# Optimization experiments

Hardware: AMD Instinct MI355X
Metric: run time of the kernel (lower is better)

Reference implementation:

```python
import jax, jax.numpy as jnp
import numpy as np

D_MODEL = 256
N_HEADS = 8
N_LEVELS = 4
N_POINTS = 4
HEAD_DIM = D_MODEL // N_HEADS
SPATIAL = [(64, 64), (32, 32), (16, 16), (8, 8)]
LEN_IN = sum(h * w for h, w in SPATIAL)
BATCH = 4
LEN_Q = LEN_IN


def _offset_bias():
    # replicate the module's _reset_parameters grid init for sampling_offsets.bias
    th = np.arange(N_HEADS, dtype=np.float64) * (2.0 * np.pi / N_HEADS)
    g = np.stack([np.cos(th), np.sin(th)], -1)
    g = g / np.abs(g).max(-1, keepdims=True)
    g = np.tile(g[:, None, None, :], (1, N_LEVELS, N_POINTS, 1))
    g = g * (np.arange(N_POINTS) + 1)[None, None, :, None]
    return jnp.asarray(g.reshape(-1), jnp.float32)


def setup_inputs() -> dict:
    key = jax.random.key(0)
    ks = jax.random.split(key, 10)
    s = 1.0 / np.sqrt(D_MODEL)
    return {
        "query": jax.random.normal(ks[0], (BATCH, LEN_Q, D_MODEL), jnp.float32),
        "reference_points": jax.random.uniform(ks[1], (BATCH, LEN_Q, N_LEVELS, 2), jnp.float32),
        "input_flatten": jax.random.normal(ks[2], (BATCH, LEN_IN, D_MODEL), jnp.float32),
        "input_spatial_shapes": np.array(SPATIAL, dtype=np.int64),
        "input_level_start_index": np.cumsum([0] + [h * w for h, w in SPATIAL[:-1]]).astype(np.int64),
        "W_val": jax.random.normal(ks[3], (D_MODEL, D_MODEL), jnp.float32) * s,
        "b_val": jnp.zeros((D_MODEL,), jnp.float32),
        "W_off": jax.random.normal(ks[4], (D_MODEL, N_HEADS * N_LEVELS * N_POINTS * 2), jnp.float32) * 0.01,
        "b_off": _offset_bias(),
        "W_attn": jax.random.normal(ks[5], (D_MODEL, N_HEADS * N_LEVELS * N_POINTS), jnp.float32) * 0.01,
        "b_attn": jnp.zeros((N_HEADS * N_LEVELS * N_POINTS,), jnp.float32),
        "W_out": jax.random.normal(ks[6], (D_MODEL, D_MODEL), jnp.float32) * s,
        "b_out": jnp.zeros((D_MODEL,), jnp.float32),
    }


def bilinear_sample(v, grid):
    # v: [B, C, H, W]; grid: [B, Q, P, 2] normalized to [-1, 1] (x=W axis, y=H axis)
    # matches torch F.grid_sample(mode='bilinear', padding_mode='zeros', align_corners=False)
    B, C, H, W = v.shape
    x = (grid[..., 0] + 1.0) * (W * 0.5) - 0.5
    y = (grid[..., 1] + 1.0) * (H * 0.5) - 0.5
    x0 = jnp.floor(x)
    y0 = jnp.floor(y)
    wx = x - x0
    wy = y - y0
    v_flat = v.reshape(B, C, H * W)

    def corner(xi, yi, wgt):
        valid = (xi >= 0) & (xi <= W - 1) & (yi >= 0) & (yi <= H - 1)
        xc = jnp.clip(xi, 0, W - 1).astype(jnp.int32)
        yc = jnp.clip(yi, 0, H - 1).astype(jnp.int32)
        idx = (yc * W + xc).reshape(B, 1, -1)
        g = jnp.take_along_axis(v_flat, jnp.broadcast_to(idx, (B, C, idx.shape[-1])), axis=2)
        return g * (wgt * valid).reshape(B, 1, -1)

    out = (corner(x0, y0, (1 - wx) * (1 - wy))
           + corner(x0 + 1, y0, wx * (1 - wy))
           + corner(x0, y0 + 1, (1 - wx) * wy)
           + corner(x0 + 1, y0 + 1, wx * wy))
    return out.reshape(B, C, grid.shape[1], grid.shape[2])


def reference(query, reference_points, input_flatten, input_spatial_shapes,
              input_level_start_index, W_val, b_val, W_off, b_off,
              W_attn, b_attn, W_out, b_out):
    ss = np.asarray(input_spatial_shapes)  # static [L, 2] (H, W)
    Nb, Lq, _ = query.shape
    value = (input_flatten @ W_val + b_val).reshape(Nb, -1, N_HEADS, HEAD_DIM)
    off = (query @ W_off + b_off).reshape(Nb, Lq, N_HEADS, N_LEVELS, N_POINTS, 2)
    attn = (query @ W_attn + b_attn).reshape(Nb, Lq, N_HEADS, N_LEVELS * N_POINTS)
    attn = jax.nn.softmax(attn, -1).reshape(Nb, Lq, N_HEADS, N_LEVELS, N_POINTS)
    # offset normalizer: (W, H) per level
    normalizer = jnp.asarray(ss[:, ::-1].copy(), jnp.float32)
    loc = reference_points[:, :, None, :, None, :] + off / normalizer[None, None, None, :, None, :]
    grids = 2.0 * loc - 1.0  # [N, Lq, H, L, P, 2]
    splits = np.cumsum([int(h) * int(w) for h, w in ss])[:-1]
    value_list = jnp.split(value, splits, axis=1)
    out = jnp.zeros((Nb * N_HEADS, HEAD_DIM, Lq), query.dtype)
    for lid, (h, w) in enumerate(ss):
        h, w = int(h), int(w)
        v = value_list[lid].transpose(0, 2, 3, 1).reshape(Nb * N_HEADS, HEAD_DIM, h, w)
        g = grids[:, :, :, lid].transpose(0, 2, 1, 3, 4).reshape(Nb * N_HEADS, Lq, N_POINTS, 2)
        sampled = bilinear_sample(v, g)  # [N*H, D, Lq, P]
        aw = attn[:, :, :, lid].transpose(0, 2, 1, 3).reshape(Nb * N_HEADS, 1, Lq, N_POINTS)
        out = out + (sampled * aw).sum(-1)
    out = out.reshape(Nb, N_HEADS * HEAD_DIM, Lq).transpose(0, 2, 1)
    return out @ W_out + b_out
```

## Files before the change

### kernel.cpp

```cpp
#include <hip/hip_runtime.h>
#include <hip/hip_bf16.h>
#include <math.h>

typedef unsigned short ushort_t;
typedef __attribute__((ext_vector_type(8))) short bf16x8;
typedef __attribute__((ext_vector_type(4))) float f32x4;

constexpr int BATCH   = 4;
constexpr int D_MODEL = 256;
constexpr int LEN_IN  = 5440;
constexpr int LEN_Q   = 5440;
constexpr int M_TOT   = BATCH * LEN_Q;

#define ASG __attribute__((address_space(1)))
#define ASL __attribute__((address_space(3)))

__device__ __forceinline__ void gld16(const void* g, void* l) {
    __builtin_amdgcn_global_load_lds((ASG const void*)g, (ASL void*)l, 16, 0, 0);
}

__device__ __forceinline__ ushort_t bfbits(float x) {
    __hip_bfloat16 h = __float2bfloat16(x);
    ushort_t u; __builtin_memcpy(&u, &h, 2); return u;
}
__device__ __forceinline__ unsigned pk2(float a, float b) {
    return (unsigned)bfbits(a) | ((unsigned)bfbits(b) << 16);
}

__global__ __launch_bounds__(256) void pack_inputs(
    const float* __restrict__ inflat, const float* __restrict__ query,
    const float* __restrict__ Wv, const float* __restrict__ Wo,
    const float* __restrict__ Wa, const float* __restrict__ Wout,
    const float* __restrict__ b_off, const float* __restrict__ b_attn,
    ushort_t* __restrict__ in_bf, ushort_t* __restrict__ q_bf,
    ushort_t* __restrict__ wvT, ushort_t* __restrict__ woaT,
    ushort_t* __restrict__ woutT, float* __restrict__ bias_oa)
{
    const int blk = blockIdx.x, tid = threadIdx.x;
    if (blk < 5440) {
        const float* src = (blk < 2720) ? inflat : query;
        ushort_t*    dst = (blk < 2720) ? in_bf : q_bf;
        const int rb = (blk < 2720) ? blk : blk - 2720;
        const size_t base = (size_t)rb * 2048 + tid * 8;
        float4 a = *(const float4*)(src + base);
        float4 b = *(const float4*)(src + base + 4);
        uint4 o;
        o.x = pk2(a.x, a.y); o.y = pk2(a.z, a.w);
        o.z = pk2(b.x, b.y); o.w = pk2(b.z, b.w);
        *(uint4*)(dst + base) = o;
    } else if (blk < 5504) {
        const float* src = (blk < 5472) ? Wv : Wout;
        ushort_t*    dst = (blk < 5472) ? wvT : woutT;
        const int base = (blk - ((blk < 5472) ? 5440 : 5472)) * 2048;
#pragma unroll
        for (int i = 0; i < 8; i++) {
            const int idx = base + i * 256 + tid;
            const int k = idx >> 8, n = idx & 255;
            dst[n * 256 + k] = bfbits(src[idx]);
        }
    } else if (blk < 5552) {
        const int base = (blk - 5504) * 2048;
#pragma unroll
        for (int i = 0; i < 8; i++) {
            const int idx = base + i * 256 + tid;
            const int k = idx / 384, j = idx - k * 384;
            const float v = (j < 256) ? Wo[k * 256 + j] : Wa[k * 128 + (j - 256)];
            woaT[j * 256 + k] = bfbits(v);
        }
    } else {
        bias_oa[tid] = b_off[tid];
        if (tid < 128) bias_oa[256 + tid] = b_attn[tid];
    }
}

template <bool OUT_BF16>
__device__ __forceinline__ void gemm_core(
    const ushort_t* __restrict__ A, const ushort_t* __restrict__ BT,
    const float* __restrict__ bias, void* __restrict__ Cp, int N,
    int bm, int bn, ushort_t* As, ushort_t* Bs)
{
    const int tid  = threadIdx.x;
    const int wave = tid >> 6, lane = tid & 63;
    const int wm = (wave >> 1) * 64, wn = (wave & 1) * 64;
    const int c0 = 2 * wave, c1 = 2 * wave + 1;
    const int kb = (lane & 3) * 8;
    const ushort_t* gA0 = A  + (size_t)(bm + c0 * 16 + (lane >> 2)) * 256 + kb;
    const ushort_t* gA1 = A  + (size_t)(bm + c1 * 16 + (lane >> 2)) * 256 + kb;
    const ushort_t* gB0 = BT + (size_t)(bn + c0 * 16 + (lane >> 2)) * 256 + kb;
    const ushort_t* gB1 = BT + (size_t)(bn + c1 * 16 + (lane >> 2)) * 256 + kb;
    ushort_t* lA0 = As + c0 * 512;
    ushort_t* lA1 = As + c1 * 512;
    ushort_t* lB0 = Bs + c0 * 512;
    ushort_t* lB1 = Bs + c1 * 512;

    f32x4 acc[4][4] = {};

    const int row = lane & 15, kg = (lane >> 4) * 8;
    for (int kt = 0; kt < 8; kt++) {
        gld16(gA0, lA0); gld16(gA1, lA1);
        gld16(gB0, lB0); gld16(gB1, lB1);
        gA0 += 32; gA1 += 32; gB0 += 32; gB1 += 32;
        __syncthreads();
        bf16x8 af[4], bfr[4];
#pragma unroll
        for (int i = 0; i < 4; i++)
            af[i] = *(const bf16x8*)(As + (wm + i * 16 + row) * 32 + kg);
#pragma unroll
        for (int j = 0; j < 4; j++)
            bfr[j] = *(const bf16x8*)(Bs + (wn + j * 16 + row) * 32 + kg);
#pragma unroll
        for (int i = 0; i < 4; i++)
#pragma unroll
            for (int j = 0; j < 4; j++)
                acc[i][j] = __builtin_amdgcn_mfma_f32_16x16x32_bf16(
                    af[i], bfr[j], acc[i][j], 0, 0, 0);
        __syncthreads();
    }

    const int col = lane & 15, rbase = (lane >> 4) * 4;
#pragma unroll
    for (int j = 0; j < 4; j++) {
        const int cc = bn + wn + j * 16 + col;
        const float bv = bias[cc];
#pragma unroll
        for (int i = 0; i < 4; i++) {
            const int rr = bm + wm + i * 16 + rbase;
#pragma unroll
            for (int r = 0; r < 4; r++) {
                const float v = acc[i][j][r] + bv;
                if (OUT_BF16) ((ushort_t*)Cp)[(size_t)(rr + r) * N + cc] = bfbits(v);
                else          ((float*)Cp)[(size_t)(rr + r) * N + cc] = v;
            }
        }
    }
}

__global__ __launch_bounds__(256) void gemm_dual(
    const ushort_t* __restrict__ in_bf, const ushort_t* __restrict__ wvT,
    const float* __restrict__ b_val, ushort_t* __restrict__ value_bf,
    const ushort_t* __restrict__ q_bf, const ushort_t* __restrict__ woaT,
    const float* __restrict__ bias_oa, float* __restrict__ offattn)
{
    __shared__ ushort_t As[128 * 32];
    __shared__ ushort_t Bs[128 * 32];
    int blk = blockIdx.x;
    if (blk < 340) {
        const int bn = (blk & 1) * 128, bm = (blk >> 1) * 128;
        gemm_core<true>(in_bf, wvT, b_val, value_bf, 256, bm, bn, As, Bs);
    } else {
        blk -= 340;
        const int bn = (blk % 3) * 128, bm = (blk / 3) * 128;
        gemm_core<false>(q_bf, woaT, bias_oa, offattn, 384, bm, bn, As, Bs);
    }
}

__global__ __launch_bounds__(256) void gemm_out(
    const ushort_t* __restrict__ mid_bf, const ushort_t* __restrict__ woutT,
    const float* __restrict__ b_out, float* __restrict__ out)
{
    __shared__ ushort_t As[128 * 32];
    __shared__ ushort_t Bs[128 * 32];
    const int bn = (blockIdx.x & 1) * 128, bm = (blockIdx.x >> 1) * 128;
    gemm_core<false>(mid_bf, woutT, b_out, out, 256, bm, bn, As, Bs);
}

__device__ __forceinline__ void acc8(float* acc, uint4 v, float w) {
    const unsigned* p = &v.x;
#pragma unroll
    for (int d = 0; d < 4; d++) {
        const unsigned u = p[d];
        const float lo = __uint_as_float(u << 16);
        const float hi = __uint_as_float(u & 0xFFFF0000u);
        acc[2 * d]     = fmaf(w, lo, acc[2 * d]);
        acc[2 * d + 1] = fmaf(w, hi, acc[2 * d + 1]);
    }
}

__global__ __launch_bounds__(256) void msda_sample_bf16(
    const ushort_t* __restrict__ value, const float* __restrict__ refp,
    const float* __restrict__ offattn, ushort_t* __restrict__ mid)
{
    constexpr int LVL_H[4]  = {64, 32, 16, 8};
    constexpr int LVL_W[4]  = {64, 32, 16, 8};
    constexpr int LVL_ST[4] = {0, 4096, 5120, 5376};

    const int tid  = threadIdx.x;
    const int bq   = blockIdx.x * 8 + (tid >> 5);
    const int b    = bq / LEN_Q;
    const int t32  = tid & 31;
    const int head = t32 >> 2;
    const int c8   = (t32 & 3) * 8;

    const float* base = offattn + (size_t)bq * 384;
    const float* lp = base + 256 + head * 16;
    float4 l0 = ((const float4*)lp)[0];
    float4 l1 = ((const float4*)lp)[1];
    float4 l2 = ((const float4*)lp)[2];
    float4 l3 = ((const float4*)lp)[3];
    float lg[16] = {l0.x, l0.y, l0.z, l0.w, l1.x, l1.y, l1.z, l1.w,
                    l2.x, l2.y, l2.z, l2.w, l3.x, l3.y, l3.z, l3.w};
    float mx = lg[0];
#pragma unroll
    for (int j = 1; j < 16; j++) mx = fmaxf(mx, lg[j]);

    const float* op = base + head * 32;
    float4 ov[8];
#pragma unroll
    for (int j = 0; j < 8; j++) ov[j] = ((const float4*)op)[j];
    const float* rp = refp + (size_t)bq * 8;
    float4 r0 = ((const float4*)rp)[0];
    float4 r1 = ((const float4*)rp)[1];
    const float rx[4] = {r0.x, r0.z, r1.x, r1.z};
    const float ry[4] = {r0.y, r0.w, r1.y, r1.w};

    const ushort_t* vbase = value + (size_t)b * LEN_IN * 256 + head * 32 + c8;

    float acc[8] = {};
    float esum = 0.f;

#pragma unroll
    for (int l = 0; l < 4; l++) {
        const int H = LVL_H[l], W = LVL_W[l], st = LVL_ST[l];
        const float fW = (float)W, fH = (float)H;
#pragma unroll
        for (int p = 0; p < 4; p++) {
            const float* o2 = &ov[l * 2].x;
            const float ox = o2[p * 2 + 0];
            const float oy = o2[p * 2 + 1];
            const float x = (rx[l] + ox / fW) * fW - 0.5f;
            const float y = (ry[l] + oy / fH) * fH - 0.5f;
            const float x0f = floorf(x), y0f = floorf(y);
            const float wx = x - x0f, wy = y - y0f;
            const int ix0 = (int)x0f, iy0 = (int)y0f;
            const int ix1 = ix0 + 1,  iy1 = iy0 + 1;
            const float vx0 = (ix0 >= 0 && ix0 < W) ? 1.f : 0.f;
            const float vx1 = (ix1 >= 0 && ix1 < W) ? 1.f : 0.f;
            const float vy0 = (iy0 >= 0 && iy0 < H) ? 1.f : 0.f;
            const float vy1 = (iy1 >= 0 && iy1 < H) ? 1.f : 0.f;
            const int cx0 = min(max(ix0, 0), W - 1);
            const int cx1 = min(max(ix1, 0), W - 1);
            const int cy0 = min(max(iy0, 0), H - 1);
            const int cy1 = min(max(iy1, 0), H - 1);
            const float hx0 = (1.f - wx) * vx0, hx1 = wx * vx1;
            const float hy0 = (1.f - wy) * vy0, hy1 = wy * vy1;

            const ushort_t* rp0 = vbase + (size_t)(st + cy0 * W) * 256;
            const ushort_t* rp1 = vbase + (size_t)(st + cy1 * W) * 256;
            uint4 v00 = *(const uint4*)(rp0 + (size_t)cx0 * 256);
            uint4 v01 = *(const uint4*)(rp0 + (size_t)cx1 * 256);
            uint4 v10 = *(const uint4*)(rp1 + (size_t)cx0 * 256);
            uint4 v11 = *(const uint4*)(rp1 + (size_t)cx1 * 256);

            const float e = __expf(lg[l * 4 + p] - mx);
            esum += e;
            acc8(acc, v00, e * hx0 * hy0);
            acc8(acc, v01, e * hx1 * hy0);
            acc8(acc, v10, e * hx0 * hy1);
            acc8(acc, v11, e * hx1 * hy1);
        }
    }

    const float inv = 1.f / esum;
    uint4 o;
    o.x = pk2(acc[0] * inv, acc[1] * inv);
    o.y = pk2(acc[2] * inv, acc[3] * inv);
    o.z = pk2(acc[4] * inv, acc[5] * inv);
    o.w = pk2(acc[6] * inv, acc[7] * inv);
    *(uint4*)(mid + (size_t)bq * 256 + head * 32 + c8) = o;
}

extern "C" void kernel_launch(void* const* d_in, const int* in_sizes, int n_in,
                              void* d_out, int out_size, void* d_ws, size_t ws_size,
                              hipStream_t stream)
{
    const float* query  = (const float*)d_in[0];
    const float* refp   = (const float*)d_in[1];
    const float* inflat = (const float*)d_in[2];
    const float* W_val  = (const float*)d_in[5];
    const float* b_val  = (const float*)d_in[6];
    const float* W_off  = (const float*)d_in[7];
    const float* W_attn = (const float*)d_in[9];
    const float* b_off  = (const float*)d_in[8];
    const float* b_attn = (const float*)d_in[10];
    const float* W_out  = (const float*)d_in[11];
    const float* b_out  = (const float*)d_in[12];
    float* out = (float*)d_out;

    char* ws = (char*)d_ws;
    ushort_t* in_bf    = (ushort_t*)ws;
    ushort_t* q_bf     = (ushort_t*)(ws + 11141120);
    ushort_t* value_bf = (ushort_t*)(ws + 22282240);
    ushort_t* wvT      = (ushort_t*)(ws + 33423360);
    ushort_t* woutT    = (ushort_t*)(ws + 33554432);
    ushort_t* woaT     = (ushort_t*)(ws + 33685504);
    float*    bias_oa  = (float*)   (ws + 33882112);
    float*    offattn  = (float*)   (ws + 33883648);
    ushort_t* mid_bf   = in_bf;

    dim3 blk(256);
    pack_inputs<<<dim3(5553), blk, 0, stream>>>(
        inflat, query, W_val, W_off, W_attn, W_out, b_off, b_attn,
        in_bf, q_bf, wvT, woaT, woutT, bias_oa);
    gemm_dual<<<dim3(850), blk, 0, stream>>>(
        in_bf, wvT, b_val, value_bf, q_bf, woaT, bias_oa, offattn);
    msda_sample_bf16<<<dim3(M_TOT / 8), blk, 0, stream>>>(
        value_bf, refp, offattn, mid_bf);
    gemm_out<<<dim3(340), blk, 0, stream>>>(
        mid_bf, woutT, b_out, out);
}
```

Before: 206.1 us.

## Fuse fp32-to-bf16 input conversion into GEMM loads, stage epilogue, prefetch samples

Drops the separate pass that converted input_flatten and query to bf16. The projection GEMM now reads the fp32 activations directly and converts them in registers before storing to LDS, using plain loads in place of global_load_lds. The GEMM epilogue is staged through LDS so each lane writes contiguous 16-element rows with vector stores, instead of scattered scalar stores. The sampling kernel is software-pipelined so the next point's four corner loads are issued before the current point is accumulated. In exchange, the GEMM reads twice as many bytes of A and uses more synchronisation barriers per tile.

```diff
diff --git a/kernel.cpp b/kernel.cpp
--- a/kernel.cpp
+++ b/kernel.cpp
@@ -7,18 +7,10 @@
 typedef __attribute__((ext_vector_type(4))) float f32x4;
 
 constexpr int BATCH   = 4;
-constexpr int D_MODEL = 256;
 constexpr int LEN_IN  = 5440;
 constexpr int LEN_Q   = 5440;
 constexpr int M_TOT   = BATCH * LEN_Q;
 
-#define ASG __attribute__((address_space(1)))
-#define ASL __attribute__((address_space(3)))
-
-__device__ __forceinline__ void gld16(const void* g, void* l) {
-    __builtin_amdgcn_global_load_lds((ASG const void*)g, (ASL void*)l, 16, 0, 0);
-}
-
 __device__ __forceinline__ ushort_t bfbits(float x) {
     __hip_bfloat16 h = __float2bfloat16(x);
     ushort_t u; __builtin_memcpy(&u, &h, 2); return u;
@@ -27,39 +19,26 @@
     return (unsigned)bfbits(a) | ((unsigned)bfbits(b) << 16);
 }
 
-__global__ __launch_bounds__(256) void pack_inputs(
-    const float* __restrict__ inflat, const float* __restrict__ query,
+__global__ __launch_bounds__(256) void pack_w(
     const float* __restrict__ Wv, const float* __restrict__ Wo,
     const float* __restrict__ Wa, const float* __restrict__ Wout,
     const float* __restrict__ b_off, const float* __restrict__ b_attn,
-    ushort_t* __restrict__ in_bf, ushort_t* __restrict__ q_bf,
     ushort_t* __restrict__ wvT, ushort_t* __restrict__ woaT,
     ushort_t* __restrict__ woutT, float* __restrict__ bias_oa)
 {
     const int blk = blockIdx.x, tid = threadIdx.x;
-    if (blk < 5440) {
-        const float* src = (blk < 2720) ? inflat : query;
-        ushort_t*    dst = (blk < 2720) ? in_bf : q_bf;
-        const int rb = (blk < 2720) ? blk : blk - 2720;
-        const size_t base = (size_t)rb * 2048 + tid * 8;
-        float4 a = *(const float4*)(src + base);
-        float4 b = *(const float4*)(src + base + 4);
-        uint4 o;
-        o.x = pk2(a.x, a.y); o.y = pk2(a.z, a.w);
-        o.z = pk2(b.x, b.y); o.w = pk2(b.z, b.w);
-        *(uint4*)(dst + base) = o;
-    } else if (blk < 5504) {
-        const float* src = (blk < 5472) ? Wv : Wout;
-        ushort_t*    dst = (blk < 5472) ? wvT : woutT;
-        const int base = (blk - ((blk < 5472) ? 5440 : 5472)) * 2048;
+    if (blk < 64) {
+        const float* src = (blk < 32) ? Wv : Wout;
+        ushort_t*    dst = (blk < 32) ? wvT : woutT;
+        const int base = (blk & 31) * 2048;
 #pragma unroll
         for (int i = 0; i < 8; i++) {
             const int idx = base + i * 256 + tid;
             const int k = idx >> 8, n = idx & 255;
             dst[n * 256 + k] = bfbits(src[idx]);
         }
-    } else if (blk < 5552) {
-        const int base = (blk - 5504) * 2048;
+    } else if (blk < 112) {
+        const int base = (blk - 64) * 2048;
 #pragma unroll
         for (int i = 0; i < 8; i++) {
             const int idx = base + i * 256 + tid;
@@ -73,84 +52,123 @@
     }
 }
 
-template <bool OUT_BF16>
+template <bool A_F32, bool OUT_BF16>
 __device__ __forceinline__ void gemm_core(
-    const ushort_t* __restrict__ A, const ushort_t* __restrict__ BT,
+    const void* __restrict__ Ap, const ushort_t* __restrict__ BT,
     const float* __restrict__ bias, void* __restrict__ Cp, int N,
-    int bm, int bn, ushort_t* As, ushort_t* Bs)
-{
+    int bm, int bn, ushort_t* SMEM)
+{
+    ushort_t* As = SMEM;
+    ushort_t* Bs = SMEM + 4096;
     const int tid  = threadIdx.x;
     const int wave = tid >> 6, lane = tid & 63;
     const int wm = (wave >> 1) * 64, wn = (wave & 1) * 64;
-    const int c0 = 2 * wave, c1 = 2 * wave + 1;
-    const int kb = (lane & 3) * 8;
-    const ushort_t* gA0 = A  + (size_t)(bm + c0 * 16 + (lane >> 2)) * 256 + kb;
-    const ushort_t* gA1 = A  + (size_t)(bm + c1 * 16 + (lane >> 2)) * 256 + kb;
-    const ushort_t* gB0 = BT + (size_t)(bn + c0 * 16 + (lane >> 2)) * 256 + kb;
-    const ushort_t* gB1 = BT + (size_t)(bn + c1 * 16 + (lane >> 2)) * 256 + kb;
-    ushort_t* lA0 = As + c0 * 512;
-    ushort_t* lA1 = As + c1 * 512;
-    ushort_t* lB0 = Bs + c0 * 512;
-    ushort_t* lB1 = Bs + c1 * 512;
+    const int srow = tid >> 1, skh = (tid & 1) * 16;
+    const int row16 = lane & 15, kg = (lane >> 4) * 8;
 
     f32x4 acc[4][4] = {};
 
-    const int row = lane & 15, kg = (lane >> 4) * 8;
     for (int kt = 0; kt < 8; kt++) {
-        gld16(gA0, lA0); gld16(gA1, lA1);
-        gld16(gB0, lB0); gld16(gB1, lB1);
-        gA0 += 32; gA1 += 32; gB0 += 32; gB1 += 32;
+        const int k0 = kt * 32;
+        uint4 a0, a1;
+        if (A_F32) {
+            const float* ap = (const float*)Ap + (size_t)(bm + srow) * 256 + k0 + skh;
+            float4 f0 = *(const float4*)(ap);
+            float4 f1 = *(const float4*)(ap + 4);
+            float4 f2 = *(const float4*)(ap + 8);
+            float4 f3 = *(const float4*)(ap + 12);
+            a0.x = pk2(f0.x, f0.y); a0.y = pk2(f0.z, f0.w);
+            a0.z = pk2(f1.x, f1.y); a0.w = pk2(f1.z, f1.w);
+            a1.x = pk2(f2.x, f2.y); a1.y = pk2(f2.z, f2.w);
+            a1.z = pk2(f3.x, f3.y); a1.w = pk2(f3.z, f3.w);
+        } else {
+            const ushort_t* ap = (const ushort_t*)Ap + (size_t)(bm + srow) * 256 + k0 + skh;
+            a0 = ((const uint4*)ap)[0];
+            a1 = ((const uint4*)ap)[1];
+        }
+        const ushort_t* bp = BT + (size_t)(bn + srow) * 256 + k0 + skh;
+        uint4 b0 = ((const uint4*)bp)[0];
+        uint4 b1 = ((const uint4*)bp)[1];
+        __syncthreads();
+        *(uint4*)(As + srow * 32 + skh)     = a0;
+        *(uint4*)(As + srow * 32 + skh + 8) = a1;
+        *(uint4*)(Bs + srow * 32 + skh)     = b0;
+        *(uint4*)(Bs + srow * 32 + skh + 8) = b1;
         __syncthreads();
         bf16x8 af[4], bfr[4];
 #pragma unroll
         for (int i = 0; i < 4; i++)
-            af[i] = *(const bf16x8*)(As + (wm + i * 16 + row) * 32 + kg);
+            af[i] = *(const bf16x8*)(As + (wm + i * 16 + row16) * 32 + kg);
 #pragma unroll
         for (int j = 0; j < 4; j++)
-            bfr[j] = *(const bf16x8*)(Bs + (wn + j * 16 + row) * 32 + kg);
+            bfr[j] = *(const bf16x8*)(Bs + (wn + j * 16 + row16) * 32 + kg);
 #pragma unroll
         for (int i = 0; i < 4; i++)
 #pragma unroll
             for (int j = 0; j < 4; j++)
                 acc[i][j] = __builtin_amdgcn_mfma_f32_16x16x32_bf16(
                     af[i], bfr[j], acc[i][j], 0, 0, 0);
+    }
+
+    float* sw = (float*)SMEM + wave * (16 * 68);
+    const int rb4 = (lane >> 4) * 4;
+    float bv[4];
+#pragma unroll
+    for (int j = 0; j < 4; j++) bv[j] = bias[bn + wn + j * 16 + row16];
+    const int err = lane >> 2;
+    const int ecs = (lane & 3) * 16;
+
+#pragma unroll
+    for (int i = 0; i < 4; i++) {
         __syncthreads();
-    }
-
-    const int col = lane & 15, rbase = (lane >> 4) * 4;
-#pragma unroll
-    for (int j = 0; j < 4; j++) {
-        const int cc = bn + wn + j * 16 + col;
-        const float bv = bias[cc];
-#pragma unroll
-        for (int i = 0; i < 4; i++) {
-            const int rr = bm + wm + i * 16 + rbase;
-#pragma unroll
-            for (int r = 0; r < 4; r++) {
-                const float v = acc[i][j][r] + bv;
-                if (OUT_BF16) ((ushort_t*)Cp)[(size_t)(rr + r) * N + cc] = bfbits(v);
-                else          ((float*)Cp)[(size_t)(rr + r) * N + cc] = v;
-            }
+#pragma unroll
+        for (int j = 0; j < 4; j++)
+#pragma unroll
+            for (int r = 0; r < 4; r++)
+                sw[(rb4 + r) * 68 + j * 16 + row16] = acc[i][j][r] + bv[j];
+        __syncthreads();
+        const float* rp = sw + err * 68 + ecs;
+        f32x4 v0 = ((const f32x4*)rp)[0];
+        f32x4 v1 = ((const f32x4*)rp)[1];
+        f32x4 v2 = ((const f32x4*)rp)[2];
+        f32x4 v3 = ((const f32x4*)rp)[3];
+        const int grow = bm + wm + i * 16 + err;
+        if (OUT_BF16) {
+            ushort_t* cp = (ushort_t*)Cp + (size_t)grow * N + bn + wn + ecs;
+            uint4 o0, o1;
+            o0.x = pk2(v0[0], v0[1]); o0.y = pk2(v0[2], v0[3]);
+            o0.z = pk2(v1[0], v1[1]); o0.w = pk2(v1[2], v1[3]);
+            o1.x = pk2(v2[0], v2[1]); o1.y = pk2(v2[2], v2[3]);
+            o1.z = pk2(v3[0], v3[1]); o1.w = pk2(v3[2], v3[3]);
+            ((uint4*)cp)[0] = o0;
+            ((uint4*)cp)[1] = o1;
+        } else {
+            float* cp = (float*)Cp + (size_t)grow * N + bn + wn + ecs;
+            ((f32x4*)cp)[0] = v0;
+            ((f32x4*)cp)[1] = v1;
+            ((f32x4*)cp)[2] = v2;
+            ((f32x4*)cp)[3] = v3;
         }
     }
 }
 
+constexpr int SMEM_USHORTS = 4 * 16 * 68 * 2;
+
 __global__ __launch_bounds__(256) void gemm_dual(
-    const ushort_t* __restrict__ in_bf, const ushort_t* __restrict__ wvT,
+    const float* __restrict__ inflat, const ushort_t* __restrict__ wvT,
     const float* __restrict__ b_val, ushort_t* __restrict__ value_bf,
-    const ushort_t* __restrict__ q_bf, const ushort_t* __restrict__ woaT,
+    const float* __restrict__ query, const ushort_t* __restrict__ woaT,
     const float* __restrict__ bias_oa, float* __restrict__ offattn)
 {
-    __shared__ ushort_t As[128 * 32];
-    __shared__ ushort_t Bs[128 * 32];
+    __shared__ ushort_t SMEM[SMEM_USHORTS];
     int blk = blockIdx.x;
     if (blk < 340) {
         const int bn = (blk & 1) * 128, bm = (blk >> 1) * 128;
-        gemm_core<true>(in_bf, wvT, b_val, value_bf, 256, bm, bn, As, Bs);
+        gemm_core<true, true>(inflat, wvT, b_val, value_bf, 256, bm, bn, SMEM);
     } else {
         blk -= 340;
         const int bn = (blk % 3) * 128, bm = (blk / 3) * 128;
-        gemm_core<false>(q_bf, woaT, bias_oa, offattn, 384, bm, bn, As, Bs);
+        gemm_core<true, false>(query, woaT, bias_oa, offattn, 384, bm, bn, SMEM);
     }
 }
 
@@ -158,10 +176,9 @@
     const ushort_t* __restrict__ mid_bf, const ushort_t* __restrict__ woutT,
     const float* __restrict__ b_out, float* __restrict__ out)
 {
-    __shared__ ushort_t As[128 * 32];
-    __shared__ ushort_t Bs[128 * 32];
+    __shared__ ushort_t SMEM[SMEM_USHORTS];
     const int bn = (blockIdx.x & 1) * 128, bm = (blockIdx.x >> 1) * 128;
-    gemm_core<false>(mid_bf, woutT, b_out, out, 256, bm, bn, As, Bs);
+    gemm_core<false, false>(mid_bf, woutT, b_out, out, 256, bm, bn, SMEM);
 }
 
 __device__ __forceinline__ void acc8(float* acc, uint4 v, float w) {
@@ -218,46 +235,62 @@
     float acc[8] = {};
     float esum = 0.f;
 
-#pragma unroll
-    for (int l = 0; l < 4; l++) {
+    int   A00[2], A01[2], A10[2], A11[2];
+    float W00[2], W01[2], W10[2], W11[2];
+    uint4 V00[2], V01[2], V10[2], V11[2];
+
+    auto comp = [&](int pi) {
+        const int s = pi & 1;
+        const int l = pi >> 2, p = pi & 3;
         const int H = LVL_H[l], W = LVL_W[l], st = LVL_ST[l];
         const float fW = (float)W, fH = (float)H;
-#pragma unroll
-        for (int p = 0; p < 4; p++) {
-            const float* o2 = &ov[l * 2].x;
-            const float ox = o2[p * 2 + 0];
-            const float oy = o2[p * 2 + 1];
-            const float x = (rx[l] + ox / fW) * fW - 0.5f;
-            const float y = (ry[l] + oy / fH) * fH - 0.5f;
-            const float x0f = floorf(x), y0f = floorf(y);
-            const float wx = x - x0f, wy = y - y0f;
-            const int ix0 = (int)x0f, iy0 = (int)y0f;
-            const int ix1 = ix0 + 1,  iy1 = iy0 + 1;
-            const float vx0 = (ix0 >= 0 && ix0 < W) ? 1.f : 0.f;
-            const float vx1 = (ix1 >= 0 && ix1 < W) ? 1.f : 0.f;
-            const float vy0 = (iy0 >= 0 && iy0 < H) ? 1.f : 0.f;
-            const float vy1 = (iy1 >= 0 && iy1 < H) ? 1.f : 0.f;
-            const int cx0 = min(max(ix0, 0), W - 1);
-            const int cx1 = min(max(ix1, 0), W - 1);
-            const int cy0 = min(max(iy0, 0), H - 1);
-            const int cy1 = min(max(iy1, 0), H - 1);
-            const float hx0 = (1.f - wx) * vx0, hx1 = wx * vx1;
-            const float hy0 = (1.f - wy) * vy0, hy1 = wy * vy1;
-
-            const ushort_t* rp0 = vbase + (size_t)(st + cy0 * W) * 256;
-            const ushort_t* rp1 = vbase + (size_t)(st + cy1 * W) * 256;
-            uint4 v00 = *(const uint4*)(rp0 + (size_t)cx0 * 256);
-            uint4 v01 = *(const uint4*)(rp0 + (size_t)cx1 * 256);
-            uint4 v10 = *(const uint4*)(rp1 + (size_t)cx0 * 256);
-            uint4 v11 = *(const uint4*)(rp1 + (size_t)cx1 * 256);
-
-            const float e = __expf(lg[l * 4 + p] - mx);
-            esum += e;
-            acc8(acc, v00, e * hx0 * hy0);
-            acc8(acc, v01, e * hx1 * hy0);
-            acc8(acc, v10, e * hx0 * hy1);
-            acc8(acc, v11, e * hx1 * hy1);
-        }
+        const float* o2 = &ov[l * 2].x;
+        const float ox = o2[p * 2 + 0];
+        const float oy = o2[p * 2 + 1];
+        const float x = (rx[l] + ox / fW) * fW - 0.5f;
+        const float y = (ry[l] + oy / fH) * fH - 0.5f;
+        const float x0f = floorf(x), y0f = floorf(y);
+        const float wx = x - x0f, wy = y - y0f;
+        const int ix0 = (int)x0f, iy0 = (int)y0f;
+        const int ix1 = ix0 + 1,  iy1 = iy0 + 1;
+        const float vx0 = (ix0 >= 0 && ix0 < W) ? 1.f : 0.f;
+        const float vx1 = (ix1 >= 0 && ix1 < W) ? 1.f : 0.f;
+        const float vy0 = (iy0 >= 0 && iy0 < H) ? 1.f : 0.f;
+        const float vy1 = (iy1 >= 0 && iy1 < H) ? 1.f : 0.f;
+        const int cx0 = min(max(ix0, 0), W - 1);
+        const int cx1 = min(max(ix1, 0), W - 1);
+        const int cy0 = min(max(iy0, 0), H - 1);
+        const int cy1 = min(max(iy1, 0), H - 1);
+        const float hx0 = (1.f - wx) * vx0, hx1 = wx * vx1;
+        const float hy0 = (1.f - wy) * vy0, hy1 = wy * vy1;
+        const int r0i = (st + cy0 * W) * 256;
+        const int r1i = (st + cy1 * W) * 256;
+        A00[s] = r0i + cx0 * 256;
+        A01[s] = r0i + cx1 * 256;
+        A10[s] = r1i + cx0 * 256;
+        A11[s] = r1i + cx1 * 256;
+        const float e = __expf(lg[pi] - mx);
+        esum += e;
+        W00[s] = e * hx0 * hy0; W01[s] = e * hx1 * hy0;
+        W10[s] = e * hx0 * hy1; W11[s] = e * hx1 * hy1;
+    };
+    auto load = [&](int pi) {
+        const int s = pi & 1;
+        V00[s] = *(const uint4*)(vbase + A00[s]);
+        V01[s] = *(const uint4*)(vbase + A01[s]);
+        V10[s] = *(const uint4*)(vbase + A10[s]);
+        V11[s] = *(const uint4*)(vbase + A11[s]);
+    };
+
+    comp(0); load(0);
+#pragma unroll
+    for (int pi = 0; pi < 16; pi++) {
+        if (pi < 15) { comp(pi + 1); load(pi + 1); }
+        const int s = pi & 1;
+        acc8(acc, V00[s], W00[s]);
+        acc8(acc, V01[s], W01[s]);
+        acc8(acc, V10[s], W10[s]);
+        acc8(acc, V11[s], W11[s]);
     }
 
     const float inv = 1.f / esum;
@@ -279,30 +312,27 @@
     const float* W_val  = (const float*)d_in[5];
     const float* b_val  = (const float*)d_in[6];
     const float* W_off  = (const float*)d_in[7];
+    const float* b_off  = (const float*)d_in[8];
     const float* W_attn = (const float*)d_in[9];
-    const float* b_off  = (const float*)d_in[8];
     const float* b_attn = (const float*)d_in[10];
     const float* W_out  = (const float*)d_in[11];
     const float* b_out  = (const float*)d_in[12];
     float* out = (float*)d_out;
 
     char* ws = (char*)d_ws;
-    ushort_t* in_bf    = (ushort_t*)ws;
-    ushort_t* q_bf     = (ushort_t*)(ws + 11141120);
-    ushort_t* value_bf = (ushort_t*)(ws + 22282240);
-    ushort_t* wvT      = (ushort_t*)(ws + 33423360);
-    ushort_t* woutT    = (ushort_t*)(ws + 33554432);
-    ushort_t* woaT     = (ushort_t*)(ws + 33685504);
-    float*    bias_oa  = (float*)   (ws + 33882112);
-    float*    offattn  = (float*)   (ws + 33883648);
-    ushort_t* mid_bf   = in_bf;
+    ushort_t* value_bf = (ushort_t*)ws;
+    ushort_t* mid_bf   = (ushort_t*)(ws + 11141120);
+    float*    offattn  = (float*)   (ws + 22282240);
+    ushort_t* wvT      = (ushort_t*)(ws + 55705600);
+    ushort_t* woutT    = (ushort_t*)(ws + 55836672);
+    ushort_t* woaT     = (ushort_t*)(ws + 55967744);
+    float*    bias_oa  = (float*)   (ws + 56164352);
 
     dim3 blk(256);
-    pack_inputs<<<dim3(5553), blk, 0, stream>>>(
-        inflat, query, W_val, W_off, W_attn, W_out, b_off, b_attn,
-        in_bf, q_bf, wvT, woaT, woutT, bias_oa);
+    pack_w<<<dim3(113), blk, 0, stream>>>(
+        W_val, W_off, W_attn, W_out, b_off, b_attn, wvT, woaT, woutT, bias_oa);
     gemm_dual<<<dim3(850), blk, 0, stream>>>(
-        in_bf, wvT, b_val, value_bf, q_bf, woaT, bias_oa, offattn);
+        inflat, wvT, b_val, value_bf, query, woaT, bias_oa, offattn);
     msda_sample_bf16<<<dim3(M_TOT / 8), blk, 0, stream>>>(
         value_bf, refp, offattn, mid_bf);
     gemm_out<<<dim3(340), blk, 0, stream>>>(
```

Measured after the change: 221.5 us. +7.5%, slower.

## Fuse fp32-to-bf16 input conversion into register-resident single-wave GEMMs

Applied to the files above, without the earlier changes.

Drops the separate pass that packed the query and input tensors to bf16, so the projection GEMMs now read fp32 activations directly and convert them in registers. The LDS-tiled 256-thread GEMM is replaced by one-wave blocks that keep a 64-column slice of the weight matrix in registers as MFMA fragments and stream over 8 row tiles. This removes a full read and write of both activation tensors and all LDS traffic and barriers. In exchange each wave reloads its weight slice, register pressure is high (two waves per SIMD requested), and the A rows are read uncoalesced from global memory.

```diff
diff --git a/kernel.cpp b/kernel.cpp
--- a/kernel.cpp
+++ b/kernel.cpp
@@ -7,18 +7,10 @@
 typedef __attribute__((ext_vector_type(4))) float f32x4;
 
 constexpr int BATCH   = 4;
-constexpr int D_MODEL = 256;
 constexpr int LEN_IN  = 5440;
 constexpr int LEN_Q   = 5440;
 constexpr int M_TOT   = BATCH * LEN_Q;
 
-#define ASG __attribute__((address_space(1)))
-#define ASL __attribute__((address_space(3)))
-
-__device__ __forceinline__ void gld16(const void* g, void* l) {
-    __builtin_amdgcn_global_load_lds((ASG const void*)g, (ASL void*)l, 16, 0, 0);
-}
-
 __device__ __forceinline__ ushort_t bfbits(float x) {
     __hip_bfloat16 h = __float2bfloat16(x);
     ushort_t u; __builtin_memcpy(&u, &h, 2); return u;
@@ -27,39 +19,26 @@
     return (unsigned)bfbits(a) | ((unsigned)bfbits(b) << 16);
 }
 
-__global__ __launch_bounds__(256) void pack_inputs(
-    const float* __restrict__ inflat, const float* __restrict__ query,
+__global__ __launch_bounds__(256) void pack_w(
     const float* __restrict__ Wv, const float* __restrict__ Wo,
     const float* __restrict__ Wa, const float* __restrict__ Wout,
     const float* __restrict__ b_off, const float* __restrict__ b_attn,
-    ushort_t* __restrict__ in_bf, ushort_t* __restrict__ q_bf,
     ushort_t* __restrict__ wvT, ushort_t* __restrict__ woaT,
     ushort_t* __restrict__ woutT, float* __restrict__ bias_oa)
 {
     const int blk = blockIdx.x, tid = threadIdx.x;
-    if (blk < 5440) {
-        const float* src = (blk < 2720) ? inflat : query;
-        ushort_t*    dst = (blk < 2720) ? in_bf : q_bf;
-        const int rb = (blk < 2720) ? blk : blk - 2720;
-        const size_t base = (size_t)rb * 2048 + tid * 8;
-        float4 a = *(const float4*)(src + base);
-        float4 b = *(const float4*)(src + base + 4);
-        uint4 o;
-        o.x = pk2(a.x, a.y); o.y = pk2(a.z, a.w);
-        o.z = pk2(b.x, b.y); o.w = pk2(b.z, b.w);
-        *(uint4*)(dst + base) = o;
-    } else if (blk < 5504) {
-        const float* src = (blk < 5472) ? Wv : Wout;
-        ushort_t*    dst = (blk < 5472) ? wvT : woutT;
-        const int base = (blk - ((blk < 5472) ? 5440 : 5472)) * 2048;
+    if (blk < 64) {
+        const float* src = (blk < 32) ? Wv : Wout;
+        ushort_t*    dst = (blk < 32) ? wvT : woutT;
+        const int base = (blk & 31) * 2048;
 #pragma unroll
         for (int i = 0; i < 8; i++) {
             const int idx = base + i * 256 + tid;
             const int k = idx >> 8, n = idx & 255;
             dst[n * 256 + k] = bfbits(src[idx]);
         }
-    } else if (blk < 5552) {
-        const int base = (blk - 5504) * 2048;
+    } else if (blk < 112) {
+        const int base = (blk - 64) * 2048;
 #pragma unroll
         for (int i = 0; i < 8; i++) {
             const int idx = base + i * 256 + tid;
@@ -73,95 +52,100 @@
     }
 }
 
-template <bool OUT_BF16>
-__device__ __forceinline__ void gemm_core(
-    const ushort_t* __restrict__ A, const ushort_t* __restrict__ BT,
+constexpr int MC = 8;
+
+template <bool A_F32, bool OUT_BF16>
+__device__ __forceinline__ void gemm_wave(
+    const void* __restrict__ Ap, const ushort_t* __restrict__ BT,
     const float* __restrict__ bias, void* __restrict__ Cp, int N,
-    int bm, int bn, ushort_t* As, ushort_t* Bs)
-{
-    const int tid  = threadIdx.x;
-    const int wave = tid >> 6, lane = tid & 63;
-    const int wm = (wave >> 1) * 64, wn = (wave & 1) * 64;
-    const int c0 = 2 * wave, c1 = 2 * wave + 1;
-    const int kb = (lane & 3) * 8;
-    const ushort_t* gA0 = A  + (size_t)(bm + c0 * 16 + (lane >> 2)) * 256 + kb;
-    const ushort_t* gA1 = A  + (size_t)(bm + c1 * 16 + (lane >> 2)) * 256 + kb;
-    const ushort_t* gB0 = BT + (size_t)(bn + c0 * 16 + (lane >> 2)) * 256 + kb;
-    const ushort_t* gB1 = BT + (size_t)(bn + c1 * 16 + (lane >> 2)) * 256 + kb;
-    ushort_t* lA0 = As + c0 * 512;
-    ushort_t* lA1 = As + c1 * 512;
-    ushort_t* lB0 = Bs + c0 * 512;
-    ushort_t* lB1 = Bs + c1 * 512;
-
-    f32x4 acc[4][4] = {};
-
-    const int row = lane & 15, kg = (lane >> 4) * 8;
-    for (int kt = 0; kt < 8; kt++) {
-        gld16(gA0, lA0); gld16(gA1, lA1);
-        gld16(gB0, lB0); gld16(gB1, lB1);
-        gA0 += 32; gA1 += 32; gB0 += 32; gB1 += 32;
-        __syncthreads();
-        bf16x8 af[4], bfr[4];
-#pragma unroll
-        for (int i = 0; i < 4; i++)
-            af[i] = *(const bf16x8*)(As + (wm + i * 16 + row) * 32 + kg);
-#pragma unroll
-        for (int j = 0; j < 4; j++)
-            bfr[j] = *(const bf16x8*)(Bs + (wn + j * 16 + row) * 32 + kg);
-#pragma unroll
-        for (int i = 0; i < 4; i++)
-#pragma unroll
-            for (int j = 0; j < 4; j++)
-                acc[i][j] = __builtin_amdgcn_mfma_f32_16x16x32_bf16(
-                    af[i], bfr[j], acc[i][j], 0, 0, 0);
-        __syncthreads();
-    }
-
-    const int col = lane & 15, rbase = (lane >> 4) * 4;
-#pragma unroll
-    for (int j = 0; j < 4; j++) {
-        const int cc = bn + wn + j * 16 + col;
-        const float bv = bias[cc];
-#pragma unroll
-        for (int i = 0; i < 4; i++) {
-            const int rr = bm + wm + i * 16 + rbase;
+    int n0, int row_base)
+{
+    const int lane  = threadIdx.x & 63;
+    const int row16 = lane & 15;
+    const int kg8   = (lane >> 4) * 8;
+    const int rb4   = (lane >> 4) * 4;
+
+    bf16x8 Bf[4][8];
+#pragma unroll
+    for (int nt = 0; nt < 4; nt++)
+#pragma unroll
+        for (int kt = 0; kt < 8; kt++)
+            Bf[nt][kt] = *(const bf16x8*)(BT + (size_t)(n0 + nt * 16 + row16) * 256
+                                             + kt * 32 + kg8);
+    float bv[4];
+#pragma unroll
+    for (int nt = 0; nt < 4; nt++) bv[nt] = bias[n0 + nt * 16 + row16];
+
+#pragma unroll 1
+    for (int mt = 0; mt < MC; mt++) {
+        const int row0 = row_base + mt * 16;
+        bf16x8 af[8];
+        if (A_F32) {
+            const float* ap = (const float*)Ap + (size_t)(row0 + row16) * 256 + kg8;
+#pragma unroll
+            for (int kt = 0; kt < 8; kt++) {
+                float4 f0 = *(const float4*)(ap + kt * 32);
+                float4 f1 = *(const float4*)(ap + kt * 32 + 4);
+                uint4 u;
+                u.x = pk2(f0.x, f0.y); u.y = pk2(f0.z, f0.w);
+                u.z = pk2(f1.x, f1.y); u.w = pk2(f1.z, f1.w);
+                __builtin_memcpy(&af[kt], &u, 16);
+            }
+        } else {
+            const ushort_t* ap = (const ushort_t*)Ap + (size_t)(row0 + row16) * 256 + kg8;
+#pragma unroll
+            for (int kt = 0; kt < 8; kt++)
+                af[kt] = *(const bf16x8*)(ap + kt * 32);
+        }
+
+        f32x4 acc[4] = {};
+#pragma unroll
+        for (int kt = 0; kt < 8; kt++)
+#pragma unroll
+            for (int nt = 0; nt < 4; nt++)
+                acc[nt] = __builtin_amdgcn_mfma_f32_16x16x32_bf16(
+                    af[kt], Bf[nt][kt], acc[nt], 0, 0, 0);
+
+#pragma unroll
+        for (int nt = 0; nt < 4; nt++) {
+            const int cc = n0 + nt * 16 + row16;
 #pragma unroll
             for (int r = 0; r < 4; r++) {
-                const float v = acc[i][j][r] + bv;
-                if (OUT_BF16) ((ushort_t*)Cp)[(size_t)(rr + r) * N + cc] = bfbits(v);
-                else          ((float*)Cp)[(size_t)(rr + r) * N + cc] = v;
+                const float v = acc[nt][r] + bv[nt];
+                const size_t ci = (size_t)(row0 + rb4 + r) * N + cc;
+                if (OUT_BF16) ((ushort_t*)Cp)[ci] = bfbits(v);
+                else          ((float*)Cp)[ci] = v;
             }
         }
     }
 }
 
-__global__ __launch_bounds__(256) void gemm_dual(
-    const ushort_t* __restrict__ in_bf, const ushort_t* __restrict__ wvT,
+__global__ __launch_bounds__(64, 2) void gemm_vo(
+    const float* __restrict__ inflat, const ushort_t* __restrict__ wvT,
     const float* __restrict__ b_val, ushort_t* __restrict__ value_bf,
-    const ushort_t* __restrict__ q_bf, const ushort_t* __restrict__ woaT,
+    const float* __restrict__ query, const ushort_t* __restrict__ woaT,
     const float* __restrict__ bias_oa, float* __restrict__ offattn)
 {
-    __shared__ ushort_t As[128 * 32];
-    __shared__ ushort_t Bs[128 * 32];
-    int blk = blockIdx.x;
-    if (blk < 340) {
-        const int bn = (blk & 1) * 128, bm = (blk >> 1) * 128;
-        gemm_core<true>(in_bf, wvT, b_val, value_bf, 256, bm, bn, As, Bs);
+    int j = blockIdx.x;
+    if (j < 680) {
+        const int s = j & 3, chunk = j >> 2;
+        gemm_wave<true, true>(inflat, wvT, b_val, value_bf, 256,
+                              s * 64, chunk * (MC * 16));
     } else {
-        blk -= 340;
-        const int bn = (blk % 3) * 128, bm = (blk / 3) * 128;
-        gemm_core<false>(q_bf, woaT, bias_oa, offattn, 384, bm, bn, As, Bs);
-    }
-}
-
-__global__ __launch_bounds__(256) void gemm_out(
+        j -= 680;
+        const int s = j % 6, chunk = j / 6;
+        gemm_wave<true, false>(query, woaT, bias_oa, offattn, 384,
+                               s * 64, chunk * (MC * 16));
+    }
+}
+
+__global__ __launch_bounds__(64, 2) void gemm_out(
     const ushort_t* __restrict__ mid_bf, const ushort_t* __restrict__ woutT,
     const float* __restrict__ b_out, float* __restrict__ out)
 {
-    __shared__ ushort_t As[128 * 32];
-    __shared__ ushort_t Bs[128 * 32];
-    const int bn = (blockIdx.x & 1) * 128, bm = (blockIdx.x >> 1) * 128;
-    gemm_core<false>(mid_bf, woutT, b_out, out, 256, bm, bn, As, Bs);
+    const int s = blockIdx.x & 3, chunk = blockIdx.x >> 2;
+    gemm_wave<false, false>(mid_bf, woutT, b_out, out, 256,
+                            s * 64, chunk * (MC * 16));
 }
 
 __device__ __forceinline__ void acc8(float* acc, uint4 v, float w) {
@@ -279,32 +263,28 @@
     const float* W_val  = (const float*)d_in[5];
     const float* b_val  = (const float*)d_in[6];
     const float* W_off  = (const float*)d_in[7];
+    const float* b_off  = (const float*)d_in[8];
     const float* W_attn = (const float*)d_in[9];
-    const float* b_off  = (const float*)d_in[8];
     const float* b_attn = (const float*)d_in[10];
     const float* W_out  = (const float*)d_in[11];
     const float* b_out  = (const float*)d_in[12];
     float* out = (float*)d_out;
 
     char* ws = (char*)d_ws;
-    ushort_t* in_bf    = (ushort_t*)ws;
-    ushort_t* q_bf     = (ushort_t*)(ws + 11141120);
-    ushort_t* value_bf = (ushort_t*)(ws + 22282240);
-    ushort_t* wvT      = (ushort_t*)(ws + 33423360);
-    ushort_t* woutT    = (ushort_t*)(ws + 33554432);
-    ushort_t* woaT     = (ushort_t*)(ws + 33685504);
-    float*    bias_oa  = (float*)   (ws + 33882112);
-    float*    offattn  = (float*)   (ws + 33883648);
-    ushort_t* mid_bf   = in_bf;
-
-    dim3 blk(256);
-    pack_inputs<<<dim3(5553), blk, 0, stream>>>(
-        inflat, query, W_val, W_off, W_attn, W_out, b_off, b_attn,
-        in_bf, q_bf, wvT, woaT, woutT, bias_oa);
-    gemm_dual<<<dim3(850), blk, 0, stream>>>(
-        in_bf, wvT, b_val, value_bf, q_bf, woaT, bias_oa, offattn);
-    msda_sample_bf16<<<dim3(M_TOT / 8), blk, 0, stream>>>(
+    ushort_t* value_bf = (ushort_t*)ws;
+    ushort_t* mid_bf   = (ushort_t*)(ws + 11141120);
+    float*    offattn  = (float*)   (ws + 22282240);
+    ushort_t* wvT      = (ushort_t*)(ws + 55705600);
+    ushort_t* woutT    = (ushort_t*)(ws + 55836672);
+    ushort_t* woaT     = (ushort_t*)(ws + 55967744);
+    float*    bias_oa  = (float*)   (ws + 56164352);
+
+    pack_w<<<dim3(113), dim3(256), 0, stream>>>(
+        W_val, W_off, W_attn, W_out, b_off, b_attn, wvT, woaT, woutT, bias_oa);
+    gemm_vo<<<dim3(1700), dim3(64), 0, stream>>>(
+        inflat, wvT, b_val, value_bf, query, woaT, bias_oa, offattn);
+    msda_sample_bf16<<<dim3(M_TOT / 8), dim3(256), 0, stream>>>(
         value_bf, refp, offattn, mid_bf);
-    gemm_out<<<dim3(340), blk, 0, stream>>>(
+    gemm_out<<<dim3(680), dim3(64), 0, stream>>>(
         mid_bf, woutT, b_out, out);
 }
```

New measurement: 222.2 us. +7.8%, slower.
